# Kernel tuning notes

Measured on AMD Instinct MI355X. Metric: run time of the kernel, lower is better.

The kernel has to match this reference:

```python
import jax, jax.numpy as jnp
import numpy as np

S, B, D, A = 8192, 64, 512, 256


def setup_inputs() -> dict:
    key = jax.random.key(0)
    ks = jax.random.split(key, 7)
    return {
        "x": jax.random.normal(ks[0], (S, B, D), dtype=jnp.float32),
        "h": jax.random.normal(ks[1], (1, B, D), dtype=jnp.float32),
        "Wx": jax.random.normal(ks[2], (A, D), dtype=jnp.float32) * (1.0 / np.sqrt(D)),
        "bx": jax.random.normal(ks[3], (A,), dtype=jnp.float32) * 0.01,
        "Wh": jax.random.normal(ks[4], (A, D), dtype=jnp.float32) * (1.0 / np.sqrt(D)),
        "Wt": jax.random.normal(ks[5], (1, A), dtype=jnp.float32) * (1.0 / np.sqrt(A)),
        "bt": jax.random.normal(ks[6], (1,), dtype=jnp.float32) * 0.01,
    }


def reference(x, h, Wx, bx, Wh, Wt, bt):
    # x: (S, B, D) seq-first; h: (1, B, D) hidden state.
    # All Conv1d ops have kernel size 1 -> plain per-position matmuls.
    xb = jnp.transpose(x, (1, 0, 2))               # (B, S, D)
    wx = jnp.einsum('bsd,ad->bas', xb, Wx) + bx[None, :, None]   # (B, A, S)
    h0 = h.transpose(1, 0, 2).reshape(-1, h.shape[-1])           # (B, D)
    wh = h0 @ Wh.T                                                # (B, A)
    # score conv (A -> 1) on tanh(wx + wh), then softmax over seq dim
    score = jnp.einsum('a,bas->bs', Wt[0], jnp.tanh(wx + wh[:, :, None])) + bt[0]  # (B, S)
    attn = jax.nn.softmax(score, axis=-1)                         # (B, S)
    out = jnp.einsum('bs,bsd->bd', attn, xb)                      # (B, D)
    return out
```

## Files before the change

kernel.cpp:

```cpp
#include <hip/hip_runtime.h>


#define S_DIM 8192
#define B_DIM 64
#define D_DIM 512
#define A_DIM 256
#define BM 64
#define BK 64
#define NCHUNK 8
#define NTILES 128

typedef _Float16 half8 __attribute__((ext_vector_type(8)));
typedef float f32x4 __attribute__((ext_vector_type(4)));

#define SMEM_MAIN (65536 + (256 + 64 + 256 + 256) * 4)

__device__ __forceinline__ float tanh_fast(float x) {
  float e = __expf(2.0f * x);
  return 1.0f - 2.0f * __builtin_amdgcn_rcpf(e + 1.0f);
}

__global__ void __launch_bounds__(256)
convw_kernel(const float* __restrict__ Wx, _Float16* __restrict__ Wp) {
  const int idx = (blockIdx.x * 256 + threadIdx.x) * 8;
  const int a = idx >> 9;
  const int k = idx & 511;
  f32x4 va = *(const f32x4*)(Wx + idx);
  f32x4 vb = *(const f32x4*)(Wx + idx + 4);
  half8 hx;
#pragma unroll
  for (int i = 0; i < 4; ++i) { hx[i] = (_Float16)va[i]; hx[4 + i] = (_Float16)vb[i]; }
  const int ta = a >> 4, fr = a & 15;
  const int tk = k >> 5, fg = (k >> 3) & 3;
  *(half8*)(Wp + (ta * 16 + tk) * 512 + (fg * 16 + fr) * 8) = hx;
}

__global__ void __launch_bounds__(256)
whb_kernel(const float* __restrict__ h, const float* __restrict__ Wh,
           const float* __restrict__ bx, float* __restrict__ whb) {
  __shared__ float hs[D_DIM];
  const int b = blockIdx.x, tid = threadIdx.x;
  hs[tid] = h[b * D_DIM + tid];
  hs[tid + 256] = h[b * D_DIM + 256 + tid];
  __syncthreads();
  const int g = tid >> 4, i = tid & 15;
  for (int pass = 0; pass < 16; ++pass) {
    const int a = pass * 16 + g;
    const f32x4* wrow = (const f32x4*)(Wh + (size_t)a * D_DIM);
    float dot = 0.f;
#pragma unroll
    for (int k = 0; k < 8; ++k) {
      f32x4 wv = wrow[i + k * 16];
      f32x4 hv = *(const f32x4*)(hs + (i + k * 16) * 4);
      dot += wv[0] * hv[0] + wv[1] * hv[1] + wv[2] * hv[2] + wv[3] * hv[3];
    }
#pragma unroll
    for (int mask = 1; mask < 16; mask <<= 1) dot += __shfl_xor(dot, mask, 64);
    if (i == 0) whb[b * A_DIM + a] = dot + bx[a];
  }
}

__global__ void __launch_bounds__(512, 4)
paa_main(const float* __restrict__ x, const _Float16* __restrict__ Wp,
         const float* __restrict__ whb, const float* __restrict__ Wt,
         float* __restrict__ m_arr, float* __restrict__ l_arr,
         float* __restrict__ acc_arr) {
  extern __shared__ char smem[];
  _Float16* xs = (_Float16*)smem;
  float* scorep = (float*)(smem + 65536);
  float* pbuf = scorep + 4 * BM;
  float* whb_s = pbuf + BM;
  float* wt_s = whb_s + A_DIM;

  const int tid = threadIdx.x;
  const int b = blockIdx.x;
  const int tile = blockIdx.y;
  const int s0 = tile * BM;

  if (tid < A_DIM) { whb_s[tid] = whb[b * A_DIM + tid]; wt_s[tid] = Wt[tid]; }

  const int xr = tid >> 3, xj = tid & 7;
  const float* xg = x + (size_t)(s0 + xr) * (B_DIM * D_DIM) + b * D_DIM + xj * 8;
  const int xj_sw = xj ^ (xr & 7);
  _Float16* xw = xs + xr * D_DIM + xj_sw * 8;

  f32x4 xa[NCHUNK], xb[NCHUNK];
#pragma unroll
  for (int c = 0; c < NCHUNK; ++c) {
    const float* p = xg + c * BK;
    xa[c] = *(const f32x4*)(p);
    xb[c] = *(const f32x4*)(p + 4);
  }
#pragma unroll
  for (int c = 0; c < NCHUNK; ++c) {
    half8 hx;
#pragma unroll
    for (int i = 0; i < 4; ++i) { hx[i] = (_Float16)xa[c][i]; hx[4 + i] = (_Float16)xb[c][i]; }
    *(half8*)(xw + c * BK) = hx;
  }
  __syncthreads();

  f32x4 acc[2][4];
#pragma unroll
  for (int i = 0; i < 2; ++i)
#pragma unroll
    for (int j = 0; j < 4; ++j) acc[i][j] = (f32x4){0.f, 0.f, 0.f, 0.f};

  const int lane = tid & 63;
  const int wv = tid >> 6;
  const int wm = wv >> 2, wn = wv & 3;
  const int fr = lane & 15, fg = lane >> 4;
  const int a_row0 = wm * 32 + fr;
  const int akey = a_row0 & 7;
  const _Float16* wp = Wp + wn * 4 * 16 * 512 + lane * 8;

#pragma unroll
  for (int c = 0; c < NCHUNK; ++c) {
#pragma unroll
    for (int kk = 0; kk < 2; ++kk) {
      const int tk = c * 2 + kk;
      const int slot = (c * 8 + kk * 4 + fg) ^ akey;
      half8 af0 = *(const half8*)(xs + a_row0 * D_DIM + slot * 8);
      half8 af1 = *(const half8*)(xs + (a_row0 + 16) * D_DIM + slot * 8);
      half8 bf0 = *(const half8*)(wp + (0 * 16 + tk) * 512);
      half8 bf1 = *(const half8*)(wp + (1 * 16 + tk) * 512);
      half8 bf2 = *(const half8*)(wp + (2 * 16 + tk) * 512);
      half8 bf3 = *(const half8*)(wp + (3 * 16 + tk) * 512);
      acc[0][0] = __builtin_amdgcn_mfma_f32_16x16x32_f16(af0, bf0, acc[0][0], 0, 0, 0);
      acc[0][1] = __builtin_amdgcn_mfma_f32_16x16x32_f16(af0, bf1, acc[0][1], 0, 0, 0);
      acc[0][2] = __builtin_amdgcn_mfma_f32_16x16x32_f16(af0, bf2, acc[0][2], 0, 0, 0);
      acc[0][3] = __builtin_amdgcn_mfma_f32_16x16x32_f16(af0, bf3, acc[0][3], 0, 0, 0);
      acc[1][0] = __builtin_amdgcn_mfma_f32_16x16x32_f16(af1, bf0, acc[1][0], 0, 0, 0);
      acc[1][1] = __builtin_amdgcn_mfma_f32_16x16x32_f16(af1, bf1, acc[1][1], 0, 0, 0);
      acc[1][2] = __builtin_amdgcn_mfma_f32_16x16x32_f16(af1, bf2, acc[1][2], 0, 0, 0);
      acc[1][3] = __builtin_amdgcn_mfma_f32_16x16x32_f16(af1, bf3, acc[1][3], 0, 0, 0);
    }
  }

  float part[2][4];
#pragma unroll
  for (int mi = 0; mi < 2; ++mi)
#pragma unroll
    for (int r = 0; r < 4; ++r) part[mi][r] = 0.f;
#pragma unroll
  for (int ni = 0; ni < 4; ++ni) {
    const int a_idx = wn * 64 + ni * 16 + fr;
    const float wt_a = wt_s[a_idx];
    const float whb_a = whb_s[a_idx];
#pragma unroll
    for (int mi = 0; mi < 2; ++mi)
#pragma unroll
      for (int r = 0; r < 4; ++r)
        part[mi][r] += wt_a * tanh_fast(acc[mi][ni][r] + whb_a);
  }
#pragma unroll
  for (int mask = 1; mask < 16; mask <<= 1) {
#pragma unroll
    for (int mi = 0; mi < 2; ++mi)
#pragma unroll
      for (int r = 0; r < 4; ++r) part[mi][r] += __shfl_xor(part[mi][r], mask, 64);
  }
  if (fr == 0) {
#pragma unroll
    for (int mi = 0; mi < 2; ++mi)
#pragma unroll
      for (int r = 0; r < 4; ++r)
        scorep[wn * BM + wm * 32 + mi * 16 + fg * 4 + r] = part[mi][r];
  }
  __syncthreads();

  if (tid < BM) {
    float sv = scorep[tid] + scorep[BM + tid] + scorep[2 * BM + tid] + scorep[3 * BM + tid];
    float m = sv;
#pragma unroll
    for (int mask = 1; mask < 64; mask <<= 1) m = fmaxf(m, __shfl_xor(m, mask, 64));
    float p = __expf(sv - m);
    float lsum = p;
#pragma unroll
    for (int mask = 1; mask < 64; mask <<= 1) lsum += __shfl_xor(lsum, mask, 64);
    pbuf[tid] = p;
    if (tid == 0) {
      m_arr[b * NTILES + tile] = m;
      l_arr[b * NTILES + tile] = lsum;
    }
  }
  __syncthreads();

  {
    float pacc[8];
#pragma unroll
    for (int j = 0; j < 8; ++j) pacc[j] = 0.f;
#pragma unroll
    for (int r = 0; r < 8; ++r) {
      const int row = wv * 8 + r;
      const float pr = pbuf[row];
      half8 v = *(const half8*)(xs + row * D_DIM + ((lane ^ (row & 7)) * 8));
#pragma unroll
      for (int j = 0; j < 8; ++j) pacc[j] += pr * (float)v[j];
    }
    __syncthreads();
    float* red = (float*)xs;
#pragma unroll
    for (int j = 0; j < 8; ++j) red[wv * 512 + lane * 8 + j] = pacc[j];
    __syncthreads();
    float s = 0.f;
#pragma unroll
    for (int w2 = 0; w2 < 8; ++w2) s += red[w2 * 512 + tid];
    acc_arr[((size_t)(b * NTILES + tile)) * D_DIM + tid] = s;
  }
}

__global__ void __launch_bounds__(512)
combine_kernel(const float* __restrict__ m_arr, const float* __restrict__ l_arr,
               const float* __restrict__ acc_arr, float* __restrict__ out) {
  __shared__ float ml[NTILES], ls[NTILES], wl[NTILES];
  const int b = blockIdx.x, tid = threadIdx.x;
  if (tid < NTILES) {
    ml[tid] = m_arr[b * NTILES + tid];
    ls[tid] = l_arr[b * NTILES + tid];
  }
  __syncthreads();
  float M = -1e30f;
  for (int i = 0; i < NTILES; ++i) M = fmaxf(M, ml[i]);
  if (tid < NTILES) wl[tid] = __expf(ml[tid] - M);
  __syncthreads();
  float L = 0.f;
  for (int i = 0; i < NTILES; ++i) L += wl[i] * ls[i];
  float sum = 0.f;
  const size_t base = (size_t)b * NTILES * D_DIM + tid;
  for (int i = 0; i < NTILES; ++i) sum += wl[i] * acc_arr[base + (size_t)i * D_DIM];
  out[b * D_DIM + tid] = sum / L;
}

extern "C" void kernel_launch(void* const* d_in, const int* in_sizes, int n_in,
                              void* d_out, int out_size, void* d_ws, size_t ws_size,
                              hipStream_t stream) {
  const float* x = (const float*)d_in[0];
  const float* h = (const float*)d_in[1];
  const float* Wx = (const float*)d_in[2];
  const float* bx = (const float*)d_in[3];
  const float* Wh = (const float*)d_in[4];
  const float* Wt = (const float*)d_in[5];

  char* ws = (char*)d_ws;
  _Float16* Wp = (_Float16*)ws;
  float* whb = (float*)(ws + 262144);
  float* m_arr = (float*)(ws + 262144 + 65536);
  float* l_arr = (float*)(ws + 262144 + 65536 + 32768);
  float* acc_arr = (float*)(ws + 262144 + 65536 + 65536);

  hipFuncSetAttribute(reinterpret_cast<const void*>(paa_main),
                      hipFuncAttributeMaxDynamicSharedMemorySize, SMEM_MAIN);

  hipLaunchKernelGGL(convw_kernel, dim3(64), dim3(256), 0, stream, Wx, Wp);
  hipLaunchKernelGGL(whb_kernel, dim3(B_DIM), dim3(256), 0, stream, h, Wh, bx, whb);
  hipLaunchKernelGGL(paa_main, dim3(B_DIM, NTILES), dim3(512), SMEM_MAIN, stream,
                     x, Wp, whb, Wt, m_arr, l_arr, acc_arr);
  hipLaunchKernelGGL(combine_kernel, dim3(B_DIM), dim3(512), 0, stream,
                     m_arr, l_arr, acc_arr, (float*)d_out);
}
```

Baseline: 405.7 us.

## Make paa_main persistent with warp-specialized double-buffered x staging

Replaces the one-tile-per-block grid (64x128 blocks) with 256 persistent blocks, each looping over 32 sequence tiles of one batch. Four waves run the MFMA score computation on the current tile, and the other four waves load and convert the next tile into a second LDS buffer. The goal is to overlap global loads of x with compute and to amortize the whb/Wt setup across tiles. In exchange, only half the waves do MFMA, LDS doubles so occupancy drops to about two blocks per CU, and each tile now needs four block-wide barriers.

```diff
diff --git a/kernel.cpp b/kernel.cpp
--- a/kernel.cpp
+++ b/kernel.cpp
@@ -6,14 +6,15 @@
 #define D_DIM 512
 #define A_DIM 256
 #define BM 64
-#define BK 64
-#define NCHUNK 8
 #define NTILES 128
-
+#define TPB 32
+#define NBLK 256
+
+typedef _Float16 half4 __attribute__((ext_vector_type(4)));
 typedef _Float16 half8 __attribute__((ext_vector_type(8)));
 typedef float f32x4 __attribute__((ext_vector_type(4)));
 
-#define SMEM_MAIN (65536 + (256 + 64 + 256 + 256) * 4)
+#define SMEM_MAIN (131072 + 16384 + 1024 + 256 + 1024 + 1024)
 
 __device__ __forceinline__ float tanh_fast(float x) {
   float e = __expf(2.0f * x);
@@ -60,153 +61,154 @@
   }
 }
 
-__global__ void __launch_bounds__(512, 4)
+template <int NR>
+__device__ __forceinline__ void stage_rows(_Float16* dst, const float* __restrict__ x,
+                                           int t_idx, int b, int r0, int lane) {
+#pragma unroll
+  for (int rr = 0; rr < NR; ++rr) {
+    const int row = r0 + rr;
+    const float* rp = x + ((size_t)(t_idx * BM + row) * B_DIM + b) * D_DIM;
+    f32x4 v0 = *(const f32x4*)(rp + lane * 4);
+    f32x4 v1 = *(const f32x4*)(rp + 256 + lane * 4);
+    half4 h0, h1;
+#pragma unroll
+    for (int j = 0; j < 4; ++j) { h0[j] = (_Float16)v0[j]; h1[j] = (_Float16)v1[j]; }
+    const int sl = (((lane >> 1) ^ (row & 7)) << 3) + ((lane & 1) << 2);
+    *(half4*)(dst + row * D_DIM + sl) = h0;
+    *(half4*)(dst + row * D_DIM + sl + 256) = h1;
+  }
+}
+
+__global__ void __launch_bounds__(512, 2)
 paa_main(const float* __restrict__ x, const _Float16* __restrict__ Wp,
          const float* __restrict__ whb, const float* __restrict__ Wt,
          float* __restrict__ m_arr, float* __restrict__ l_arr,
          float* __restrict__ acc_arr) {
   extern __shared__ char smem[];
-  _Float16* xs = (_Float16*)smem;
-  float* scorep = (float*)(smem + 65536);
-  float* pbuf = scorep + 4 * BM;
-  float* whb_s = pbuf + BM;
-  float* wt_s = whb_s + A_DIM;
+  _Float16* xs0 = (_Float16*)smem;
+  _Float16* xs1 = (_Float16*)(smem + 65536);
+  float* red    = (float*)(smem + 131072);
+  float* scorep = (float*)(smem + 131072 + 16384);
+  float* pbuf   = scorep + 256;
+  float* whb_s  = pbuf + 64;
+  float* wt_s   = whb_s + 256;
 
   const int tid = threadIdx.x;
-  const int b = blockIdx.x;
-  const int tile = blockIdx.y;
-  const int s0 = tile * BM;
-
-  if (tid < A_DIM) { whb_s[tid] = whb[b * A_DIM + tid]; wt_s[tid] = Wt[tid]; }
-
-  const int xr = tid >> 3, xj = tid & 7;
-  const float* xg = x + (size_t)(s0 + xr) * (B_DIM * D_DIM) + b * D_DIM + xj * 8;
-  const int xj_sw = xj ^ (xr & 7);
-  _Float16* xw = xs + xr * D_DIM + xj_sw * 8;
-
-  f32x4 xa[NCHUNK], xb[NCHUNK];
-#pragma unroll
-  for (int c = 0; c < NCHUNK; ++c) {
-    const float* p = xg + c * BK;
-    xa[c] = *(const f32x4*)(p);
-    xb[c] = *(const f32x4*)(p + 4);
-  }
-#pragma unroll
-  for (int c = 0; c < NCHUNK; ++c) {
-    half8 hx;
-#pragma unroll
-    for (int i = 0; i < 4; ++i) { hx[i] = (_Float16)xa[c][i]; hx[4 + i] = (_Float16)xb[c][i]; }
-    *(half8*)(xw + c * BK) = hx;
-  }
-  __syncthreads();
-
-  f32x4 acc[2][4];
-#pragma unroll
-  for (int i = 0; i < 2; ++i)
-#pragma unroll
-    for (int j = 0; j < 4; ++j) acc[i][j] = (f32x4){0.f, 0.f, 0.f, 0.f};
-
   const int lane = tid & 63;
   const int wv = tid >> 6;
-  const int wm = wv >> 2, wn = wv & 3;
+  const int b = blockIdx.x >> 2;
+  const int sgrp = blockIdx.x & 3;
+
+  if (tid < A_DIM) { whb_s[tid] = whb[b * A_DIM + tid]; wt_s[tid] = Wt[tid]; }
+
   const int fr = lane & 15, fg = lane >> 4;
-  const int a_row0 = wm * 32 + fr;
-  const int akey = a_row0 & 7;
-  const _Float16* wp = Wp + wn * 4 * 16 * 512 + lane * 8;
-
-#pragma unroll
-  for (int c = 0; c < NCHUNK; ++c) {
-#pragma unroll
-    for (int kk = 0; kk < 2; ++kk) {
-      const int tk = c * 2 + kk;
-      const int slot = (c * 8 + kk * 4 + fg) ^ akey;
-      half8 af0 = *(const half8*)(xs + a_row0 * D_DIM + slot * 8);
-      half8 af1 = *(const half8*)(xs + (a_row0 + 16) * D_DIM + slot * 8);
-      half8 bf0 = *(const half8*)(wp + (0 * 16 + tk) * 512);
-      half8 bf1 = *(const half8*)(wp + (1 * 16 + tk) * 512);
-      half8 bf2 = *(const half8*)(wp + (2 * 16 + tk) * 512);
-      half8 bf3 = *(const half8*)(wp + (3 * 16 + tk) * 512);
-      acc[0][0] = __builtin_amdgcn_mfma_f32_16x16x32_f16(af0, bf0, acc[0][0], 0, 0, 0);
-      acc[0][1] = __builtin_amdgcn_mfma_f32_16x16x32_f16(af0, bf1, acc[0][1], 0, 0, 0);
-      acc[0][2] = __builtin_amdgcn_mfma_f32_16x16x32_f16(af0, bf2, acc[0][2], 0, 0, 0);
-      acc[0][3] = __builtin_amdgcn_mfma_f32_16x16x32_f16(af0, bf3, acc[0][3], 0, 0, 0);
-      acc[1][0] = __builtin_amdgcn_mfma_f32_16x16x32_f16(af1, bf0, acc[1][0], 0, 0, 0);
-      acc[1][1] = __builtin_amdgcn_mfma_f32_16x16x32_f16(af1, bf1, acc[1][1], 0, 0, 0);
-      acc[1][2] = __builtin_amdgcn_mfma_f32_16x16x32_f16(af1, bf2, acc[1][2], 0, 0, 0);
-      acc[1][3] = __builtin_amdgcn_mfma_f32_16x16x32_f16(af1, bf3, acc[1][3], 0, 0, 0);
-    }
-  }
-
-  float part[2][4];
-#pragma unroll
-  for (int mi = 0; mi < 2; ++mi)
-#pragma unroll
-    for (int r = 0; r < 4; ++r) part[mi][r] = 0.f;
-#pragma unroll
-  for (int ni = 0; ni < 4; ++ni) {
-    const int a_idx = wn * 64 + ni * 16 + fr;
-    const float wt_a = wt_s[a_idx];
-    const float whb_a = whb_s[a_idx];
-#pragma unroll
-    for (int mi = 0; mi < 2; ++mi)
-#pragma unroll
-      for (int r = 0; r < 4; ++r)
-        part[mi][r] += wt_a * tanh_fast(acc[mi][ni][r] + whb_a);
-  }
-#pragma unroll
-  for (int mask = 1; mask < 16; mask <<= 1) {
-#pragma unroll
-    for (int mi = 0; mi < 2; ++mi)
-#pragma unroll
-      for (int r = 0; r < 4; ++r) part[mi][r] += __shfl_xor(part[mi][r], mask, 64);
-  }
-  if (fr == 0) {
-#pragma unroll
-    for (int mi = 0; mi < 2; ++mi)
-#pragma unroll
-      for (int r = 0; r < 4; ++r)
-        scorep[wn * BM + wm * 32 + mi * 16 + fg * 4 + r] = part[mi][r];
-  }
-  __syncthreads();
-
-  if (tid < BM) {
-    float sv = scorep[tid] + scorep[BM + tid] + scorep[2 * BM + tid] + scorep[3 * BM + tid];
-    float m = sv;
-#pragma unroll
-    for (int mask = 1; mask < 64; mask <<= 1) m = fmaxf(m, __shfl_xor(m, mask, 64));
-    float p = __expf(sv - m);
-    float lsum = p;
-#pragma unroll
-    for (int mask = 1; mask < 64; mask <<= 1) lsum += __shfl_xor(lsum, mask, 64);
-    pbuf[tid] = p;
-    if (tid == 0) {
-      m_arr[b * NTILES + tile] = m;
-      l_arr[b * NTILES + tile] = lsum;
-    }
-  }
-  __syncthreads();
-
-  {
-    float pacc[8];
-#pragma unroll
-    for (int j = 0; j < 8; ++j) pacc[j] = 0.f;
-#pragma unroll
-    for (int r = 0; r < 8; ++r) {
-      const int row = wv * 8 + r;
-      const float pr = pbuf[row];
-      half8 v = *(const half8*)(xs + row * D_DIM + ((lane ^ (row & 7)) * 8));
-#pragma unroll
-      for (int j = 0; j < 8; ++j) pacc[j] += pr * (float)v[j];
-    }
-    __syncthreads();
-    float* red = (float*)xs;
-#pragma unroll
-    for (int j = 0; j < 8; ++j) red[wv * 512 + lane * 8 + j] = pacc[j];
-    __syncthreads();
-    float s = 0.f;
-#pragma unroll
-    for (int w2 = 0; w2 < 8; ++w2) s += red[w2 * 512 + tid];
-    acc_arr[((size_t)(b * NTILES + tile)) * D_DIM + tid] = s;
+  const _Float16* wpb = Wp + (wv & 3) * (4 * 16 * 512) + lane * 8;
+
+  stage_rows<8>(xs0, x, sgrp * TPB, b, wv * 8, lane);
+  __syncthreads();
+
+  for (int i = 0; i < TPB; ++i) {
+    const int t_idx = sgrp * TPB + i;
+    _Float16* xcur = (i & 1) ? xs1 : xs0;
+    _Float16* xnxt = (i & 1) ? xs0 : xs1;
+
+    if (wv < 4) {
+      f32x4 acc[4][4];
+#pragma unroll
+      for (int mf = 0; mf < 4; ++mf)
+#pragma unroll
+        for (int nf = 0; nf < 4; ++nf) acc[mf][nf] = (f32x4){0.f, 0.f, 0.f, 0.f};
+#pragma unroll
+      for (int tk = 0; tk < 16; ++tk) {
+        const int slot = ((tk * 4 + fg) ^ (fr & 7)) * 8;
+        half8 af[4], bf[4];
+#pragma unroll
+        for (int mf = 0; mf < 4; ++mf)
+          af[mf] = *(const half8*)(xcur + (mf * 16 + fr) * D_DIM + slot);
+#pragma unroll
+        for (int nf = 0; nf < 4; ++nf)
+          bf[nf] = *(const half8*)(wpb + (nf * 16 + tk) * 512);
+#pragma unroll
+        for (int mf = 0; mf < 4; ++mf)
+#pragma unroll
+          for (int nf = 0; nf < 4; ++nf)
+            acc[mf][nf] = __builtin_amdgcn_mfma_f32_16x16x32_f16(af[mf], bf[nf], acc[mf][nf], 0, 0, 0);
+      }
+      float part[4][4];
+#pragma unroll
+      for (int mf = 0; mf < 4; ++mf)
+#pragma unroll
+        for (int r = 0; r < 4; ++r) part[mf][r] = 0.f;
+#pragma unroll
+      for (int nf = 0; nf < 4; ++nf) {
+        const int a_idx = (wv & 3) * 64 + nf * 16 + fr;
+        const float wt_a = wt_s[a_idx];
+        const float whb_a = whb_s[a_idx];
+#pragma unroll
+        for (int mf = 0; mf < 4; ++mf)
+#pragma unroll
+          for (int r = 0; r < 4; ++r)
+            part[mf][r] += wt_a * tanh_fast(acc[mf][nf][r] + whb_a);
+      }
+#pragma unroll
+      for (int mask = 1; mask < 16; mask <<= 1)
+#pragma unroll
+        for (int mf = 0; mf < 4; ++mf)
+#pragma unroll
+          for (int r = 0; r < 4; ++r) part[mf][r] += __shfl_xor(part[mf][r], mask, 64);
+      if (fr == 0) {
+#pragma unroll
+        for (int mf = 0; mf < 4; ++mf)
+#pragma unroll
+          for (int r = 0; r < 4; ++r)
+            scorep[(wv & 3) * 64 + mf * 16 + fg * 4 + r] = part[mf][r];
+      }
+    } else if (i + 1 < TPB) {
+      stage_rows<16>(xnxt, x, t_idx + 1, b, (wv - 4) * 16, lane);
+    }
+    __syncthreads();
+
+    if (tid < BM) {
+      float sv = scorep[tid] + scorep[64 + tid] + scorep[128 + tid] + scorep[192 + tid];
+      float m = sv;
+#pragma unroll
+      for (int mask = 1; mask < 64; mask <<= 1) m = fmaxf(m, __shfl_xor(m, mask, 64));
+      float p = __expf(sv - m);
+      float lsum = p;
+#pragma unroll
+      for (int mask = 1; mask < 64; mask <<= 1) lsum += __shfl_xor(lsum, mask, 64);
+      pbuf[tid] = p;
+      if (tid == 0) {
+        m_arr[b * NTILES + t_idx] = m;
+        l_arr[b * NTILES + t_idx] = lsum;
+      }
+    }
+    __syncthreads();
+
+    {
+      float pacc[8];
+#pragma unroll
+      for (int j = 0; j < 8; ++j) pacc[j] = 0.f;
+#pragma unroll
+      for (int r = 0; r < 8; ++r) {
+        const int row = wv * 8 + r;
+        const float pr = pbuf[row];
+        half8 v = *(const half8*)(xcur + row * D_DIM + ((lane ^ (row & 7)) * 8));
+#pragma unroll
+        for (int j = 0; j < 8; ++j) pacc[j] += pr * (float)v[j];
+      }
+#pragma unroll
+      for (int j = 0; j < 8; ++j) red[wv * 512 + lane * 8 + j] = pacc[j];
+    }
+    __syncthreads();
+
+    {
+      float s = 0.f;
+#pragma unroll
+      for (int w2 = 0; w2 < 8; ++w2) s += red[w2 * 512 + tid];
+      acc_arr[((size_t)(b * NTILES + t_idx)) * D_DIM + tid] = s;
+    }
+    __syncthreads();
   }
 }
 
@@ -254,7 +256,7 @@
 
   hipLaunchKernelGGL(convw_kernel, dim3(64), dim3(256), 0, stream, Wx, Wp);
   hipLaunchKernelGGL(whb_kernel, dim3(B_DIM), dim3(256), 0, stream, h, Wh, bx, whb);
-  hipLaunchKernelGGL(paa_main, dim3(B_DIM, NTILES), dim3(512), SMEM_MAIN, stream,
+  hipLaunchKernelGGL(paa_main, dim3(NBLK), dim3(512), SMEM_MAIN, stream,
                      x, Wp, whb, Wt, m_arr, l_arr, acc_arr);
   hipLaunchKernelGGL(combine_kernel, dim3(B_DIM), dim3(512), 0, stream,
                      m_arr, l_arr, acc_arr, (float*)d_out);
```

Measured after the change: 671.9 us. 1.66x slower.

## Halve sequence tile to 32 rows with 256-thread blocks and shuffle-based reductions

Applied to the files above, without the earlier changes.

Shrinks the per-block sequence tile from 64 to 32 rows, doubling the tile count, and runs 256 threads per block, each wave owning 64 attention columns. Shared memory drops to 32 KB of static storage, intended to raise occupancy and give more blocks for latency hiding. The softmax and the weighted x-sum now use wave shuffles instead of extra shared buffers and syncs, and whb/Wt are read straight into registers. The cost is that each Wp fragment is reused over fewer rows, so weight loads per row double, and the combine kernel now has twice as many partials to reduce.

```diff
diff --git a/kernel.cpp b/kernel.cpp
--- a/kernel.cpp
+++ b/kernel.cpp
@@ -5,15 +5,11 @@
 #define B_DIM 64
 #define D_DIM 512
 #define A_DIM 256
-#define BM 64
-#define BK 64
-#define NCHUNK 8
-#define NTILES 128
+#define BM 32
+#define NTILES 256
 
 typedef _Float16 half8 __attribute__((ext_vector_type(8)));
 typedef float f32x4 __attribute__((ext_vector_type(4)));
-
-#define SMEM_MAIN (65536 + (256 + 64 + 256 + 256) * 4)
 
 __device__ __forceinline__ float tanh_fast(float x) {
   float e = __expf(2.0f * x);
@@ -60,153 +56,155 @@
   }
 }
 
-__global__ void __launch_bounds__(512, 4)
+__global__ void __launch_bounds__(256, 4)
 paa_main(const float* __restrict__ x, const _Float16* __restrict__ Wp,
          const float* __restrict__ whb, const float* __restrict__ Wt,
          float* __restrict__ m_arr, float* __restrict__ l_arr,
          float* __restrict__ acc_arr) {
-  extern __shared__ char smem[];
-  _Float16* xs = (_Float16*)smem;
-  float* scorep = (float*)(smem + 65536);
-  float* pbuf = scorep + 4 * BM;
-  float* whb_s = pbuf + BM;
-  float* wt_s = whb_s + A_DIM;
+  __shared__ _Float16 xs[BM * D_DIM];
+  __shared__ float scorep[4 * BM];
 
   const int tid = threadIdx.x;
+  const int lane = tid & 63;
+  const int wv = tid >> 6;
   const int b = blockIdx.x;
   const int tile = blockIdx.y;
-  const int s0 = tile * BM;
-
-  if (tid < A_DIM) { whb_s[tid] = whb[b * A_DIM + tid]; wt_s[tid] = Wt[tid]; }
-
-  const int xr = tid >> 3, xj = tid & 7;
-  const float* xg = x + (size_t)(s0 + xr) * (B_DIM * D_DIM) + b * D_DIM + xj * 8;
-  const int xj_sw = xj ^ (xr & 7);
-  _Float16* xw = xs + xr * D_DIM + xj_sw * 8;
-
-  f32x4 xa[NCHUNK], xb[NCHUNK];
-#pragma unroll
-  for (int c = 0; c < NCHUNK; ++c) {
-    const float* p = xg + c * BK;
-    xa[c] = *(const f32x4*)(p);
-    xb[c] = *(const f32x4*)(p + 4);
-  }
-#pragma unroll
-  for (int c = 0; c < NCHUNK; ++c) {
-    half8 hx;
-#pragma unroll
-    for (int i = 0; i < 4; ++i) { hx[i] = (_Float16)xa[c][i]; hx[4 + i] = (_Float16)xb[c][i]; }
-    *(half8*)(xw + c * BK) = hx;
+
+  const int fr = lane & 15, fg = lane >> 4;
+  const int akey = fr & 7;
+  const _Float16* wp = Wp + wv * (4 * 16 * 512) + lane * 8;
+
+  float wt_a[4], whb_a[4];
+#pragma unroll
+  for (int nf = 0; nf < 4; ++nf) {
+    wt_a[nf]  = Wt[wv * 64 + nf * 16 + fr];
+    whb_a[nf] = whb[b * A_DIM + wv * 64 + nf * 16 + fr];
+  }
+
+  const int srow = tid >> 3, sseg = tid & 7;
+  const int skey = srow & 7;
+  {
+    const float* rp = x + ((size_t)(tile * BM + srow) * B_DIM + b) * D_DIM;
+    f32x4 sa[4], sb[4];
+#pragma unroll
+    for (int p = 0; p < 4; ++p) {
+      sa[p] = *(const f32x4*)(rp + p * 64 + sseg * 8);
+      sb[p] = *(const f32x4*)(rp + p * 64 + sseg * 8 + 4);
+    }
+#pragma unroll
+    for (int p = 0; p < 4; ++p) {
+      half8 hx;
+#pragma unroll
+      for (int j = 0; j < 4; ++j) { hx[j] = (_Float16)sa[p][j]; hx[4 + j] = (_Float16)sb[p][j]; }
+      const int ch = p * 8 + sseg;
+      *(half8*)(xs + srow * D_DIM + ((ch ^ skey) * 8)) = hx;
+    }
+#pragma unroll
+    for (int p = 0; p < 4; ++p) {
+      sa[p] = *(const f32x4*)(rp + (4 + p) * 64 + sseg * 8);
+      sb[p] = *(const f32x4*)(rp + (4 + p) * 64 + sseg * 8 + 4);
+    }
+#pragma unroll
+    for (int p = 0; p < 4; ++p) {
+      half8 hx;
+#pragma unroll
+      for (int j = 0; j < 4; ++j) { hx[j] = (_Float16)sa[p][j]; hx[4 + j] = (_Float16)sb[p][j]; }
+      const int ch = (4 + p) * 8 + sseg;
+      *(half8*)(xs + srow * D_DIM + ((ch ^ skey) * 8)) = hx;
+    }
   }
   __syncthreads();
 
   f32x4 acc[2][4];
 #pragma unroll
-  for (int i = 0; i < 2; ++i)
-#pragma unroll
-    for (int j = 0; j < 4; ++j) acc[i][j] = (f32x4){0.f, 0.f, 0.f, 0.f};
-
-  const int lane = tid & 63;
-  const int wv = tid >> 6;
-  const int wm = wv >> 2, wn = wv & 3;
-  const int fr = lane & 15, fg = lane >> 4;
-  const int a_row0 = wm * 32 + fr;
-  const int akey = a_row0 & 7;
-  const _Float16* wp = Wp + wn * 4 * 16 * 512 + lane * 8;
-
-#pragma unroll
-  for (int c = 0; c < NCHUNK; ++c) {
-#pragma unroll
-    for (int kk = 0; kk < 2; ++kk) {
-      const int tk = c * 2 + kk;
-      const int slot = (c * 8 + kk * 4 + fg) ^ akey;
-      half8 af0 = *(const half8*)(xs + a_row0 * D_DIM + slot * 8);
-      half8 af1 = *(const half8*)(xs + (a_row0 + 16) * D_DIM + slot * 8);
-      half8 bf0 = *(const half8*)(wp + (0 * 16 + tk) * 512);
-      half8 bf1 = *(const half8*)(wp + (1 * 16 + tk) * 512);
-      half8 bf2 = *(const half8*)(wp + (2 * 16 + tk) * 512);
-      half8 bf3 = *(const half8*)(wp + (3 * 16 + tk) * 512);
-      acc[0][0] = __builtin_amdgcn_mfma_f32_16x16x32_f16(af0, bf0, acc[0][0], 0, 0, 0);
-      acc[0][1] = __builtin_amdgcn_mfma_f32_16x16x32_f16(af0, bf1, acc[0][1], 0, 0, 0);
-      acc[0][2] = __builtin_amdgcn_mfma_f32_16x16x32_f16(af0, bf2, acc[0][2], 0, 0, 0);
-      acc[0][3] = __builtin_amdgcn_mfma_f32_16x16x32_f16(af0, bf3, acc[0][3], 0, 0, 0);
-      acc[1][0] = __builtin_amdgcn_mfma_f32_16x16x32_f16(af1, bf0, acc[1][0], 0, 0, 0);
-      acc[1][1] = __builtin_amdgcn_mfma_f32_16x16x32_f16(af1, bf1, acc[1][1], 0, 0, 0);
-      acc[1][2] = __builtin_amdgcn_mfma_f32_16x16x32_f16(af1, bf2, acc[1][2], 0, 0, 0);
-      acc[1][3] = __builtin_amdgcn_mfma_f32_16x16x32_f16(af1, bf3, acc[1][3], 0, 0, 0);
-    }
-  }
-
-  float part[2][4];
-#pragma unroll
   for (int mi = 0; mi < 2; ++mi)
 #pragma unroll
-    for (int r = 0; r < 4; ++r) part[mi][r] = 0.f;
-#pragma unroll
-  for (int ni = 0; ni < 4; ++ni) {
-    const int a_idx = wn * 64 + ni * 16 + fr;
-    const float wt_a = wt_s[a_idx];
-    const float whb_a = whb_s[a_idx];
+    for (int nf = 0; nf < 4; ++nf) acc[mi][nf] = (f32x4){0.f, 0.f, 0.f, 0.f};
+#pragma unroll
+  for (int tk = 0; tk < 16; ++tk) {
+    const int slot = ((tk * 4 + fg) ^ akey) * 8;
+    half8 af0 = *(const half8*)(xs + (fr) * D_DIM + slot);
+    half8 af1 = *(const half8*)(xs + (16 + fr) * D_DIM + slot);
+    half8 bf0 = *(const half8*)(wp + (0 * 16 + tk) * 512);
+    half8 bf1 = *(const half8*)(wp + (1 * 16 + tk) * 512);
+    half8 bf2 = *(const half8*)(wp + (2 * 16 + tk) * 512);
+    half8 bf3 = *(const half8*)(wp + (3 * 16 + tk) * 512);
+    acc[0][0] = __builtin_amdgcn_mfma_f32_16x16x32_f16(af0, bf0, acc[0][0], 0, 0, 0);
+    acc[0][1] = __builtin_amdgcn_mfma_f32_16x16x32_f16(af0, bf1, acc[0][1], 0, 0, 0);
+    acc[0][2] = __builtin_amdgcn_mfma_f32_16x16x32_f16(af0, bf2, acc[0][2], 0, 0, 0);
+    acc[0][3] = __builtin_amdgcn_mfma_f32_16x16x32_f16(af0, bf3, acc[0][3], 0, 0, 0);
+    acc[1][0] = __builtin_amdgcn_mfma_f32_16x16x32_f16(af1, bf0, acc[1][0], 0, 0, 0);
+    acc[1][1] = __builtin_amdgcn_mfma_f32_16x16x32_f16(af1, bf1, acc[1][1], 0, 0, 0);
+    acc[1][2] = __builtin_amdgcn_mfma_f32_16x16x32_f16(af1, bf2, acc[1][2], 0, 0, 0);
+    acc[1][3] = __builtin_amdgcn_mfma_f32_16x16x32_f16(af1, bf3, acc[1][3], 0, 0, 0);
+  }
+
+  {
+    float part[2][4];
 #pragma unroll
     for (int mi = 0; mi < 2; ++mi)
 #pragma unroll
-      for (int r = 0; r < 4; ++r)
-        part[mi][r] += wt_a * tanh_fast(acc[mi][ni][r] + whb_a);
-  }
-#pragma unroll
-  for (int mask = 1; mask < 16; mask <<= 1) {
-#pragma unroll
-    for (int mi = 0; mi < 2; ++mi)
-#pragma unroll
-      for (int r = 0; r < 4; ++r) part[mi][r] += __shfl_xor(part[mi][r], mask, 64);
-  }
-  if (fr == 0) {
-#pragma unroll
-    for (int mi = 0; mi < 2; ++mi)
-#pragma unroll
-      for (int r = 0; r < 4; ++r)
-        scorep[wn * BM + wm * 32 + mi * 16 + fg * 4 + r] = part[mi][r];
-  }
-  __syncthreads();
-
-  if (tid < BM) {
-    float sv = scorep[tid] + scorep[BM + tid] + scorep[2 * BM + tid] + scorep[3 * BM + tid];
-    float m = sv;
-#pragma unroll
-    for (int mask = 1; mask < 64; mask <<= 1) m = fmaxf(m, __shfl_xor(m, mask, 64));
-    float p = __expf(sv - m);
-    float lsum = p;
-#pragma unroll
-    for (int mask = 1; mask < 64; mask <<= 1) lsum += __shfl_xor(lsum, mask, 64);
-    pbuf[tid] = p;
-    if (tid == 0) {
-      m_arr[b * NTILES + tile] = m;
-      l_arr[b * NTILES + tile] = lsum;
-    }
-  }
-  __syncthreads();
+      for (int r = 0; r < 4; ++r) part[mi][r] = 0.f;
+#pragma unroll
+    for (int nf = 0; nf < 4; ++nf)
+#pragma unroll
+      for (int mi = 0; mi < 2; ++mi)
+#pragma unroll
+        for (int r = 0; r < 4; ++r)
+          part[mi][r] += wt_a[nf] * tanh_fast(acc[mi][nf][r] + whb_a[nf]);
+#pragma unroll
+    for (int mask = 1; mask < 16; mask <<= 1)
+#pragma unroll
+      for (int mi = 0; mi < 2; ++mi)
+#pragma unroll
+        for (int r = 0; r < 4; ++r) part[mi][r] += __shfl_xor(part[mi][r], mask, 64);
+    if (fr == 0) {
+#pragma unroll
+      for (int mi = 0; mi < 2; ++mi)
+#pragma unroll
+        for (int r = 0; r < 4; ++r)
+          scorep[wv * BM + mi * 16 + fg * 4 + r] = part[mi][r];
+    }
+  }
+  __syncthreads();
+
+  const int rl = lane & 31;
+  float sv = scorep[rl] + scorep[BM + rl] + scorep[2 * BM + rl] + scorep[3 * BM + rl];
+  float m = sv;
+#pragma unroll
+  for (int mask = 1; mask < 32; mask <<= 1) m = fmaxf(m, __shfl_xor(m, mask, 64));
+  float p = __expf(sv - m);
+  float lsum = p;
+#pragma unroll
+  for (int mask = 1; mask < 32; mask <<= 1) lsum += __shfl_xor(lsum, mask, 64);
+  if (tid == 0) {
+    m_arr[b * NTILES + tile] = m;
+    l_arr[b * NTILES + tile] = lsum;
+  }
 
   {
-    float pacc[8];
-#pragma unroll
-    for (int j = 0; j < 8; ++j) pacc[j] = 0.f;
-#pragma unroll
-    for (int r = 0; r < 8; ++r) {
-      const int row = wv * 8 + r;
-      const float pr = pbuf[row];
-      half8 v = *(const half8*)(xs + row * D_DIM + ((lane ^ (row & 7)) * 8));
-#pragma unroll
-      for (int j = 0; j < 8; ++j) pacc[j] += pr * (float)v[j];
-    }
-    __syncthreads();
-    float* red = (float*)xs;
-#pragma unroll
-    for (int j = 0; j < 8; ++j) red[wv * 512 + lane * 8 + j] = pacc[j];
-    __syncthreads();
-    float s = 0.f;
-#pragma unroll
-    for (int w2 = 0; w2 < 8; ++w2) s += red[w2 * 512 + tid];
-    acc_arr[((size_t)(b * NTILES + tile)) * D_DIM + tid] = s;
+    const int q = lane >> 4;
+    const int ch = wv * 16 + (lane & 15);
+    float wacc[8];
+#pragma unroll
+    for (int j = 0; j < 8; ++j) wacc[j] = 0.f;
+#pragma unroll
+    for (int k = 0; k < 8; ++k) {
+      const int row = q * 8 + k;
+      const float pr = __shfl(p, row, 64);
+      half8 xv = *(const half8*)(xs + row * D_DIM + ((ch ^ (row & 7)) * 8));
+#pragma unroll
+      for (int j = 0; j < 8; ++j) wacc[j] += pr * (float)xv[j];
+    }
+#pragma unroll
+    for (int j = 0; j < 8; ++j) wacc[j] += __shfl_xor(wacc[j], 16, 64);
+#pragma unroll
+    for (int j = 0; j < 8; ++j) wacc[j] += __shfl_xor(wacc[j], 32, 64);
+    if (lane < 16) {
+      float* ob = acc_arr + ((size_t)(b * NTILES + tile)) * D_DIM + ch * 8;
+      *(f32x4*)(ob) = (f32x4){wacc[0], wacc[1], wacc[2], wacc[3]};
+      *(f32x4*)(ob + 4) = (f32x4){wacc[4], wacc[5], wacc[6], wacc[7]};
+    }
   }
 }
 
@@ -246,15 +244,12 @@
   _Float16* Wp = (_Float16*)ws;
   float* whb = (float*)(ws + 262144);
   float* m_arr = (float*)(ws + 262144 + 65536);
-  float* l_arr = (float*)(ws + 262144 + 65536 + 32768);
-  float* acc_arr = (float*)(ws + 262144 + 65536 + 65536);
-
-  hipFuncSetAttribute(reinterpret_cast<const void*>(paa_main),
-                      hipFuncAttributeMaxDynamicSharedMemorySize, SMEM_MAIN);
+  float* l_arr = (float*)(ws + 262144 + 65536 + 65536);
+  float* acc_arr = (float*)(ws + 262144 + 3 * 65536);
 
   hipLaunchKernelGGL(convw_kernel, dim3(64), dim3(256), 0, stream, Wx, Wp);
   hipLaunchKernelGGL(whb_kernel, dim3(B_DIM), dim3(256), 0, stream, h, Wh, bx, whb);
-  hipLaunchKernelGGL(paa_main, dim3(B_DIM, NTILES), dim3(512), SMEM_MAIN, stream,
+  hipLaunchKernelGGL(paa_main, dim3(B_DIM, NTILES), dim3(256), 0, stream,
                      x, Wp, whb, Wt, m_arr, l_arr, acc_arr);
   hipLaunchKernelGGL(combine_kernel, dim3(B_DIM), dim3(512), 0, stream,
                      m_arr, l_arr, acc_arr, (float*)d_out);
```

Result: faster. 368.0 us (-9.3%).
